# Performance work log

Hardware: AMD Instinct MI355X
Metric: run time of the kernel (lower is better)

Reference implementation:

```python
import jax, jax.numpy as jnp
import numpy as np

EPS = 1e-5

def _ln(t, g, b):
    m = t.mean(-1, keepdims=True)
    v = ((t - m) ** 2).mean(-1, keepdims=True)
    return (t - m) * jax.lax.rsqrt(v + EPS) * g + b

def _sr(t, w, b, H, W, sr):
    # t: [B, H*W, C] -> spatial-reduction conv -> [B, (H//sr)*(W//sr), C]
    B, L, C = t.shape
    xi = t.transpose(0, 2, 1).reshape(B, C, H, W)
    y = jax.lax.conv_general_dilated(xi, w, (sr, sr), 'VALID',
                                     dimension_numbers=('NCHW', 'OIHW', 'NCHW'))
    return y.reshape(B, C, -1).transpose(0, 2, 1) + b

def setup_inputs() -> dict:
    key = jax.random.key(0)
    ks = jax.random.split(key, 9)
    C, head, sr, H, W = 128, 2, 2, 64, 64
    B, N = 4, 2 * H * W
    s = 0.02
    return {
        'x': jax.random.normal(ks[0], (B, N, C), jnp.float32),
        'qW': jax.random.normal(ks[1], (C, C), jnp.float32) * s,
        'qb': jnp.zeros((C,), jnp.float32),
        'kvW': jax.random.normal(ks[2], (C, 2 * C), jnp.float32) * s,
        'kvb': jnp.zeros((2 * C,), jnp.float32),
        'projW': jax.random.normal(ks[3], (C, C), jnp.float32) * s,
        'projb': jnp.zeros((C,), jnp.float32),
        'srW': jax.random.normal(ks[4], (C, C, sr, sr), jnp.float32) * s,
        'srb': jnp.zeros((C,), jnp.float32),
        'lnW': jnp.ones((C,), jnp.float32),
        'lnB': jnp.zeros((C,), jnp.float32),
        'H': H, 'W': W, 'fuse': 1,
    }

def reference(x, qW, qb, kvW, kvb, projW, projb, srW, srb, lnW, lnB, H, W, fuse):
    head, sr = 2, 2
    B, N, C = x.shape
    Dh = C // head
    scale = Dh ** -0.5
    q = (x @ qW + qb).reshape(B, N, head, Dh).transpose(0, 2, 1, 3)  # [B,h,N,Dh]
    mask = None
    if fuse and sr > 1:
        half = N // 2
        x_rgb = _ln(_sr(x[:, :half, :], srW, srb, H, W, sr), lnW, lnB)
        x_dte = _ln(_sr(x[:, half:, :], srW, srb, H, W, sr), lnW, lnB)
        xkv = jnp.concatenate([x_rgb, x_dte], axis=1)
        M = N // (sr * sr)
        row = jnp.arange(N)[:, None] < half            # query in rgb half
        col = jnp.arange(M)[None, :] < (M // 2)        # key in rgb half
        mask = row == col                              # True on same-modality blocks -> masked
    elif sr > 1:
        xkv = _ln(_sr(x, srW, srb, H, W, sr), lnW, lnB)
    else:
        xkv = x
    M = xkv.shape[1]
    kv = (xkv @ kvW + kvb).reshape(B, M, 2, head, Dh).transpose(2, 0, 3, 1, 4)
    k, v = kv[0], kv[1]                                # [B,h,M,Dh]
    attn = jnp.einsum('bhnd,bhmd->bhnm', q, k) * scale
    if mask is not None:
        attn = jnp.where(mask[None, None], -jnp.inf, attn)
    attn = jax.nn.softmax(attn, axis=-1)
    out = jnp.einsum('bhnm,bhmd->bhnd', attn, v).transpose(0, 2, 1, 3).reshape(B, N, C)
    return out @ projW + projb
```

## Files before the change

### kernel.cpp

```cpp
#include <hip/hip_runtime.h>
#include <hip/hip_bf16.h>

#define LN_EPS 1e-5f

typedef __attribute__((ext_vector_type(8))) short bf16x8_t;
typedef __attribute__((ext_vector_type(4))) float f32x4_t;
typedef __attribute__((ext_vector_type(4))) unsigned short u16x4_t;

#define MFMA32(a, b, c) __builtin_amdgcn_mfma_f32_16x16x32_bf16(a, b, c, 0, 0, 0)

__device__ inline float fast_exp2(float x) {
#if __has_builtin(__builtin_amdgcn_exp2f)
    return __builtin_amdgcn_exp2f(x);
#else
    float r;
    asm volatile("v_exp_f32 %0, %1\n\ts_nop 0" : "=v"(r) : "v"(x));
    return r;
#endif
}

__device__ inline unsigned short f2bf(float f) {
    union { float f; unsigned int u; } v; v.f = f;
    unsigned int r = v.u + 0x7fffu + ((v.u >> 16) & 1u);
    return (unsigned short)(r >> 16);
}

__device__ inline u16x4_t pk4(float a, float b, float c, float d) {
    union { u16x4_t v; __hip_bfloat162 h[2]; } u;
    u.h[0] = __float22bfloat162_rn(float2{a, b});
    u.h[1] = __float22bfloat162_rn(float2{c, d});
    return u.v;
}
__device__ inline bf16x8_t pk8(float4 a, float4 b) {
    union { bf16x8_t v; __hip_bfloat162 h[4]; } u;
    u.h[0] = __float22bfloat162_rn(float2{a.x, a.y});
    u.h[1] = __float22bfloat162_rn(float2{a.z, a.w});
    u.h[2] = __float22bfloat162_rn(float2{b.x, b.y});
    u.h[3] = __float22bfloat162_rn(float2{b.z, b.w});
    return u.v;
}

__device__ inline size_t fragidx(int row, int k, int KC) {
    return ((size_t)((row >> 4) * KC + (k >> 5))) * 512 +
           (((k >> 3) & 3) * 16 + (row & 15)) * 8 + (k & 7);
}

__global__ void k_prep_w(const float* __restrict__ qW, const float* __restrict__ kvW,
                         const float* __restrict__ projW, const float* __restrict__ srW,
                         unsigned short* __restrict__ qWs, unsigned short* __restrict__ kvWs,
                         unsigned short* __restrict__ projWs, unsigned short* __restrict__ srWs) {
    int i = blockIdx.x * 256 + threadIdx.x;
    if (i < 16384) {
        int n = i & 127, k = i >> 7;
        qWs[fragidx(n, k, 4)] = f2bf(qW[k * 128 + n]);
    } else if (i < 49152) {
        int j = i - 16384; int n = j & 255, k = j >> 8;
        kvWs[fragidx(n, k, 4)] = f2bf(kvW[k * 256 + n]);
    } else if (i < 65536) {
        int j = i - 49152; int n = j & 127, k = j >> 7;
        projWs[fragidx(n, k, 4)] = f2bf(projW[k * 128 + n]);
    } else {
        int j = i - 65536; int n = j >> 9, rem = j & 511, q = rem >> 7, c = rem & 127;
        srWs[fragidx(n, q * 128 + c, 16)] = f2bf(srW[n * 512 + c * 4 + q]);
    }
}

#define XPAD 132
__global__ __launch_bounds__(256)
void k_convkv(const float* __restrict__ x, const unsigned short* __restrict__ srWs,
              const float* __restrict__ srb, const float* __restrict__ lnW,
              const float* __restrict__ lnB, const unsigned short* __restrict__ kvWs,
              const float* __restrict__ kvb, unsigned short* __restrict__ ksw,
              unsigned short* __restrict__ vls) {
    const int t = threadIdx.x, w = t >> 6, lane = t & 63;
    const int col = lane & 15, quad = lane >> 4;
    const int RT = blockIdx.x;

    __shared__ unsigned short xl[64 * XPAD];
    __shared__ unsigned short xs[4 * 512];
    __shared__ float lnred[4][16][2];

    const int pb = RT >> 7, phf = (RT >> 6) & 1;
    const int oy = (RT >> 1) & 31, ox0 = (RT & 1) * 16;
    const int n0 = phf * 4096 + 2 * oy * 64 + 2 * ox0;
    #pragma unroll
    for (int it = 0; it < 8; it++) {
        int idx = it * 256 + t;
        int chunk = idx >> 10;
        int rr = (idx >> 5) & 31;
        int c4 = idx & 31;
        float4 v = *(const float4*)(x + ((size_t)(pb * 8192 + n0 + chunk * 64 + rr)) * 128 + c4 * 4);
        *(u16x4_t*)(xl + (chunk * 32 + rr) * XPAD + c4 * 4) = pk4(v.x, v.y, v.z, v.w);
    }
    __syncthreads();

    f32x4_t acc[2] = {};
    {
        const unsigned short* wp = srWs + lane * 8;
        #pragma unroll
        for (int kc = 0; kc < 16; kc++) {
            const int q = kc >> 2, cg = kc & 3;
            const int r = (q >> 1) * 32 + 2 * col + (q & 1);
            bf16x8_t xb = *(const bf16x8_t*)(xl + r * XPAD + cg * 32 + quad * 8);
            #pragma unroll
            for (int jj = 0; jj < 2; jj++) {
                bf16x8_t wf = *(const bf16x8_t*)(wp + (size_t)((w * 2 + jj) * 16 + kc) * 512);
                acc[jj] = MFMA32(wf, xb, acc[jj]);
            }
        }
    }
    float s = 0.f, ss = 0.f;
    #pragma unroll
    for (int jj = 0; jj < 2; jj++) {
        float4 bs = *(const float4*)(srb + (w * 2 + jj) * 16 + quad * 4);
        acc[jj][0] += bs.x; acc[jj][1] += bs.y; acc[jj][2] += bs.z; acc[jj][3] += bs.w;
        #pragma unroll
        for (int r = 0; r < 4; r++) { float v = acc[jj][r]; s += v; ss += v * v; }
    }
    s += __shfl_xor(s, 16, 64);  s += __shfl_xor(s, 32, 64);
    ss += __shfl_xor(ss, 16, 64); ss += __shfl_xor(ss, 32, 64);
    if (lane < 16) { lnred[w][lane][0] = s; lnred[w][lane][1] = ss; }
    __syncthreads();
    float stot = 0.f, sstot = 0.f;
    #pragma unroll
    for (int ww = 0; ww < 4; ww++) { stot += lnred[ww][col][0]; sstot += lnred[ww][col][1]; }
    float mean = stot * (1.0f / 128.0f);
    float var = sstot * (1.0f / 128.0f) - mean * mean;
    float rs = rsqrtf(var + LN_EPS);
    #pragma unroll
    for (int jj = 0; jj < 2; jj++) {
        int f0 = (w * 2 + jj) * 16 + quad * 4;
        float4 g = *(const float4*)(lnW + f0);
        float4 be = *(const float4*)(lnB + f0);
        u16x4_t o = pk4((acc[jj][0] - mean) * rs * g.x + be.x,
                        (acc[jj][1] - mean) * rs * g.y + be.y,
                        (acc[jj][2] - mean) * rs * g.z + be.z,
                        (acc[jj][3] - mean) * rs * g.w + be.w);
        *(u16x4_t*)(xs + ((size_t)(f0 >> 5)) * 512 +
                    (((f0 >> 3) & 3) * 16 + col) * 8 + (f0 & 7)) = o;
    }
    __syncthreads();
    bf16x8_t xf[4];
    #pragma unroll
    for (int kc = 0; kc < 4; kc++)
        xf[kc] = *(const bf16x8_t*)(xs + (size_t)kc * 512 + lane * 8);
    const int p0 = RT * 16;
    const int bb = p0 >> 11;
    #pragma unroll
    for (int jj = 0; jj < 2; jj++) {
        const int nt = w * 2 + jj;
        f32x4_t aK = {};
        #pragma unroll
        for (int kc = 0; kc < 4; kc++) {
            bf16x8_t wf = *(const bf16x8_t*)(kvWs + (size_t)(nt * 4 + kc) * 512 + lane * 8);
            aK = MFMA32(wf, xf[kc], aK);
        }
        float4 bs = *(const float4*)(kvb + nt * 16 + quad * 4);
        int m = (p0 + col) & 2047;
        int bh = bb * 2 + (nt >> 2);
        int d0 = (nt & 3) * 16 + quad * 4;
        u16x4_t o = pk4(aK[0] + bs.x, aK[1] + bs.y, aK[2] + bs.z, aK[3] + bs.w);
        *(u16x4_t*)(ksw + ((size_t)(bh * 128 + (m >> 4)) * 2 + (d0 >> 5)) * 512 +
                    (((d0 >> 3) & 3) * 16 + (m & 15)) * 8 + (d0 & 7)) = o;
    }
    #pragma unroll
    for (int jj = 0; jj < 2; jj++) {
        const int nt = w * 2 + jj;
        f32x4_t aV = {};
        #pragma unroll
        for (int kc = 0; kc < 4; kc++) {
            bf16x8_t wf = *(const bf16x8_t*)(kvWs + (size_t)((8 + nt) * 4 + kc) * 512 + lane * 8);
            aV = MFMA32(xf[kc], wf, aV);
        }
        int fv = nt * 16 + col;
        int h = fv >> 6, dd = fv & 63;
        float bv = kvb[128 + fv];
        int m0 = (p0 + quad * 4) & 2047;
        int bh = bb * 2 + h;
        int kt = m0 >> 6;
        int tt = (m0 >> 5) & 1;
        int base = m0 & 31;
        int quad_b = base >> 3, j0 = base & 7;
        u16x4_t o = pk4(aV[0] + bv, aV[1] + bv, aV[2] + bv, aV[3] + bv);
        *(u16x4_t*)(vls + (((size_t)((bh * 32 + kt) * 4 + (dd >> 4)) * 2 + tt) * 512) +
                    (quad_b * 16 + (dd & 15)) * 8 + j0) = o;
    }
}

__global__ __launch_bounds__(256, 2)
void k_attn_f7(const float* __restrict__ x, const unsigned short* __restrict__ qWs,
               const float* __restrict__ qb, const unsigned short* __restrict__ ksw,
               const unsigned short* __restrict__ vls, const unsigned short* __restrict__ projWs,
               const float* __restrict__ projb, float* __restrict__ out) {
    const int blkx = blockIdx.x, mod = blockIdx.y, b = blockIdx.z;
    const int t = threadIdx.x, w = t >> 6, lane = t & 63;
    const int col = lane & 15, quad = lane >> 4;
    const int qg = w & 1, h = w >> 1;
    const int bh = b * 2 + h;
    const int qbase = mod * 4096 + blkx * 64 + qg * 32;

    __shared__ unsigned short sbuf[64 * 136];
    __shared__ unsigned short pls[4][2048];

    unsigned short* qarea = sbuf + w * 2048;
    const float sc = 0.125f * 1.44269504089f;
    #pragma unroll
    for (int qt = 0; qt < 2; qt++) {
        const float* xrow = x + ((size_t)b * 8192 + qbase + qt * 16 + col) * 128;
        f32x4_t acc[4] = {};
        #pragma unroll
        for (int kc = 0; kc < 4; kc++) {
            float4 xa = *(const float4*)(xrow + kc * 32 + quad * 8);
            float4 xb2 = *(const float4*)(xrow + kc * 32 + quad * 8 + 4);
            bf16x8_t xf = pk8(xa, xb2);
            #pragma unroll
            for (int j = 0; j < 4; j++) {
                bf16x8_t wf = *(const bf16x8_t*)(qWs + (size_t)((h * 4 + j) * 4 + kc) * 512 + lane * 8);
                acc[j] = MFMA32(wf, xf, acc[j]);
            }
        }
        #pragma unroll
        for (int j = 0; j < 4; j++) {
            float4 bs = *(const float4*)(qb + h * 64 + j * 16 + quad * 4);
            u16x4_t o = pk4((acc[j][0] + bs.x) * sc, (acc[j][1] + bs.y) * sc,
                            (acc[j][2] + bs.z) * sc, (acc[j][3] + bs.w) * sc);
            *(u16x4_t*)(qarea + ((size_t)(qt * 2 + (j >> 1))) * 512 +
                        (((j & 1) * 2 + (quad >> 1)) * 16 + col) * 8 + (quad & 1) * 4) = o;
        }
    }
    bf16x8_t qf[2][2];
    #pragma unroll
    for (int qt = 0; qt < 2; qt++)
        #pragma unroll
        for (int kc = 0; kc < 2; kc++)
            qf[qt][kc] = *(const bf16x8_t*)(qarea + (size_t)(qt * 2 + kc) * 512 + lane * 8);
    __syncthreads();

    const unsigned short* kp0 =
        ksw + ((size_t)(bh * 128 + (1 - mod) * 64) * 2) * 512 + lane * 8;
    const unsigned short* vp0 =
        vls + ((size_t)((bh * 32 + (1 - mod) * 16) * 8)) * 512 + lane * 8;
    const bf16x8_t ones8 = { 0x3F80, 0x3F80, 0x3F80, 0x3F80,
                             0x3F80, 0x3F80, 0x3F80, 0x3F80 };
    unsigned short* parea = pls[w];

    f32x4_t O[2][4] = {};
    f32x4_t accl[2] = {};

    bf16x8_t kf0[8], kf1[8], vf0[8], vf1[8];

    auto pref0 = [&](int kt) {
        #pragma unroll
        for (int i = 0; i < 8; i++) {
            kf0[i] = *(const bf16x8_t*)(kp0 + (size_t)(kt * 8 + i) * 512);
            vf0[i] = *(const bf16x8_t*)(vp0 + (size_t)(kt * 8 + i) * 512);
        }
    };
    auto pref1 = [&](int kt) {
        #pragma unroll
        for (int i = 0; i < 8; i++) {
            kf1[i] = *(const bf16x8_t*)(kp0 + (size_t)(kt * 8 + i) * 512);
            vf1[i] = *(const bf16x8_t*)(vp0 + (size_t)(kt * 8 + i) * 512);
        }
    };
    auto body = [&](bf16x8_t (&kfc)[8], bf16x8_t (&vfc)[8]) {
        f32x4_t ST[2][4];
        #pragma unroll
        for (int qt = 0; qt < 2; qt++)
            #pragma unroll
            for (int nb = 0; nb < 4; nb++) {
                f32x4_t sA = {};
                sA = MFMA32(kfc[nb * 2 + 0], qf[qt][0], sA);
                sA = MFMA32(kfc[nb * 2 + 1], qf[qt][1], sA);
                ST[qt][nb] = sA;
            }
        #pragma unroll
        for (int qt = 0; qt < 2; qt++)
            #pragma unroll
            for (int nb = 0; nb < 4; nb++) {
                u16x4_t pk = pk4(fast_exp2(ST[qt][nb][0]), fast_exp2(ST[qt][nb][1]),
                                 fast_exp2(ST[qt][nb][2]), fast_exp2(ST[qt][nb][3]));
                *(u16x4_t*)(parea + qt * 1024 + (nb >> 1) * 512 +
                            (((nb & 1) * 2 + (quad >> 1)) * 16 + col) * 8 + (quad & 1) * 4) = pk;
            }
        bf16x8_t pf[2][2];
        #pragma unroll
        for (int qt = 0; qt < 2; qt++) {
            pf[qt][0] = *(const bf16x8_t*)(parea + qt * 1024 + lane * 8);
            pf[qt][1] = *(const bf16x8_t*)(parea + qt * 1024 + 512 + lane * 8);
        }
        #pragma unroll
        for (int qt = 0; qt < 2; qt++) {
            accl[qt] = MFMA32(pf[qt][0], ones8, accl[qt]);
            accl[qt] = MFMA32(pf[qt][1], ones8, accl[qt]);
            #pragma unroll
            for (int dt = 0; dt < 4; dt++) {
                O[qt][dt] = MFMA32(pf[qt][0], vfc[dt * 2 + 0], O[qt][dt]);
                O[qt][dt] = MFMA32(pf[qt][1], vfc[dt * 2 + 1], O[qt][dt]);
            }
        }
    };

    pref0(0);
    #pragma unroll
    for (int kt2 = 0; kt2 < 8; kt2++) {
        pref1(kt2 * 2 + 1);
        body(kf0, vf0);
        if (kt2 < 7) pref0(kt2 * 2 + 2);
        body(kf1, vf1);
    }

    #pragma unroll
    for (int qt = 0; qt < 2; qt++) {
        #pragma unroll
        for (int r = 0; r < 4; r++) {
            float rl = 1.0f / accl[qt][r];
            int qrow = qg * 32 + qt * 16 + quad * 4 + r;
            #pragma unroll
            for (int dt = 0; dt < 4; dt++)
                sbuf[qrow * 136 + h * 64 + dt * 16 + col] = f2bf(O[qt][dt][r] * rl);
        }
    }
    __syncthreads();
    {
        const int qt2 = w;
        bf16x8_t ob[4];
        #pragma unroll
        for (int kc = 0; kc < 4; kc++)
            ob[kc] = *(const bf16x8_t*)(sbuf + (size_t)(qt2 * 16 + col) * 136 + kc * 32 + quad * 8);
        f32x4_t acc[8];
        #pragma unroll
        for (int j = 0; j < 8; j++) acc[j] = f32x4_t{};
        #pragma unroll
        for (int kc = 0; kc < 4; kc++)
            #pragma unroll
            for (int j = 0; j < 8; j++) {
                bf16x8_t wf = *(const bf16x8_t*)(projWs + (size_t)(j * 4 + kc) * 512 + lane * 8);
                acc[j] = MFMA32(wf, ob[kc], acc[j]);
            }
        const int n = b * 8192 + mod * 4096 + blkx * 64 + qt2 * 16 + col;
        #pragma unroll
        for (int j = 0; j < 8; j++) {
            int f0 = j * 16 + quad * 4;
            float4 bs = *(const float4*)(projb + f0);
            float4 o = { acc[j][0] + bs.x, acc[j][1] + bs.y,
                         acc[j][2] + bs.z, acc[j][3] + bs.w };
            *(float4*)(out + (size_t)n * 128 + f0) = o;
        }
    }
}

extern "C" void kernel_launch(void* const* d_in, const int* in_sizes, int n_in,
                              void* d_out, int out_size, void* d_ws, size_t ws_size,
                              hipStream_t stream) {
    const float* x     = (const float*)d_in[0];
    const float* qW    = (const float*)d_in[1];
    const float* qb    = (const float*)d_in[2];
    const float* kvW   = (const float*)d_in[3];
    const float* kvb   = (const float*)d_in[4];
    const float* projW = (const float*)d_in[5];
    const float* projb = (const float*)d_in[6];
    const float* srW   = (const float*)d_in[7];
    const float* srb   = (const float*)d_in[8];
    const float* lnW   = (const float*)d_in[9];
    const float* lnB   = (const float*)d_in[10];

    char* ws = (char*)d_ws;
    unsigned short* qWs    = (unsigned short*)(ws + 0);
    unsigned short* kvWs   = (unsigned short*)(ws + 32768);
    unsigned short* projWs = (unsigned short*)(ws + 98304);
    unsigned short* srWs   = (unsigned short*)(ws + 131072);
    unsigned short* ksw    = (unsigned short*)(ws + 262144);
    unsigned short* vls    = (unsigned short*)(ws + 2359296);

    k_prep_w<<<dim3(512), dim3(256), 0, stream>>>(qW, kvW, projW, srW,
                                                  qWs, kvWs, projWs, srWs);
    k_convkv<<<dim3(512), dim3(256), 0, stream>>>(x, srWs, srb, lnW, lnB,
                                                  kvWs, kvb, ksw, vls);
    k_attn_f7<<<dim3(64, 2, 4), dim3(256), 0, stream>>>(x, qWs, qb, ksw, vls,
                                                        projWs, projb, (float*)d_out);
}
```

Before: 132.3 us.

## Split key range across warps and combine partial attention outputs in LDS

Each warp now processes all 64 queries of its block for one head, but only half of the key tiles, instead of 32 queries over all keys. The two partial outputs and row sums are merged through shared memory before normalisation and the output projection. This halves the K/V fragment loads per warp and reuses each loaded K/V tile across twice as many queries. In exchange it drops the explicit double-buffered prefetch, adds LDS traffic and extra barriers for the merge, and raises register and LDS use, which may lower occupancy.

```diff
diff --git a/kernel.cpp b/kernel.cpp
--- a/kernel.cpp
+++ b/kernel.cpp
@@ -188,24 +188,26 @@
 }
 
 __global__ __launch_bounds__(256, 2)
-void k_attn_f7(const float* __restrict__ x, const unsigned short* __restrict__ qWs,
+void k_attn_f8(const float* __restrict__ x, const unsigned short* __restrict__ qWs,
                const float* __restrict__ qb, const unsigned short* __restrict__ ksw,
                const unsigned short* __restrict__ vls, const unsigned short* __restrict__ projWs,
                const float* __restrict__ projb, float* __restrict__ out) {
     const int blkx = blockIdx.x, mod = blockIdx.y, b = blockIdx.z;
     const int t = threadIdx.x, w = t >> 6, lane = t & 63;
     const int col = lane & 15, quad = lane >> 4;
-    const int qg = w & 1, h = w >> 1;
+    const int ks = w & 1, h = w >> 1;
     const int bh = b * 2 + h;
-    const int qbase = mod * 4096 + blkx * 64 + qg * 32;
+    const int qbase = mod * 4096 + blkx * 64;
 
     __shared__ unsigned short sbuf[64 * 136];
-    __shared__ unsigned short pls[4][2048];
-
-    unsigned short* qarea = sbuf + w * 2048;
+    __shared__ unsigned short pls[4][4096];
+    __shared__ float Ocomb[64 * 68];
+    __shared__ float lcomb[64];
+
     const float sc = 0.125f * 1.44269504089f;
     #pragma unroll
-    for (int qt = 0; qt < 2; qt++) {
+    for (int qtl = 0; qtl < 2; qtl++) {
+        const int qt = ks * 2 + qtl;
         const float* xrow = x + ((size_t)b * 8192 + qbase + qt * 16 + col) * 128;
         f32x4_t acc[4] = {};
         #pragma unroll
@@ -224,16 +226,18 @@
             float4 bs = *(const float4*)(qb + h * 64 + j * 16 + quad * 4);
             u16x4_t o = pk4((acc[j][0] + bs.x) * sc, (acc[j][1] + bs.y) * sc,
                             (acc[j][2] + bs.z) * sc, (acc[j][3] + bs.w) * sc);
-            *(u16x4_t*)(qarea + ((size_t)(qt * 2 + (j >> 1))) * 512 +
+            *(u16x4_t*)(sbuf + (size_t)h * 4096 + ((size_t)(qt * 2 + (j >> 1))) * 512 +
                         (((j & 1) * 2 + (quad >> 1)) * 16 + col) * 8 + (quad & 1) * 4) = o;
         }
     }
-    bf16x8_t qf[2][2];
-    #pragma unroll
-    for (int qt = 0; qt < 2; qt++)
+    __syncthreads();
+    bf16x8_t qf[4][2];
+    #pragma unroll
+    for (int qt = 0; qt < 4; qt++)
         #pragma unroll
         for (int kc = 0; kc < 2; kc++)
-            qf[qt][kc] = *(const bf16x8_t*)(qarea + (size_t)(qt * 2 + kc) * 512 + lane * 8);
+            qf[qt][kc] = *(const bf16x8_t*)(sbuf + (size_t)h * 4096 +
+                                            (size_t)(qt * 2 + kc) * 512 + lane * 8);
     __syncthreads();
 
     const unsigned short* kp0 =
@@ -244,84 +248,89 @@
                              0x3F80, 0x3F80, 0x3F80, 0x3F80 };
     unsigned short* parea = pls[w];
 
-    f32x4_t O[2][4] = {};
-    f32x4_t accl[2] = {};
-
-    bf16x8_t kf0[8], kf1[8], vf0[8], vf1[8];
-
-    auto pref0 = [&](int kt) {
+    f32x4_t O[4][4] = {};
+    f32x4_t accl[4] = {};
+
+    for (int kti = 0; kti < 8; kti++) {
+        const int kt = ks * 8 + kti;
+        bf16x8_t kf[8], vf[8];
         #pragma unroll
         for (int i = 0; i < 8; i++) {
-            kf0[i] = *(const bf16x8_t*)(kp0 + (size_t)(kt * 8 + i) * 512);
-            vf0[i] = *(const bf16x8_t*)(vp0 + (size_t)(kt * 8 + i) * 512);
-        }
-    };
-    auto pref1 = [&](int kt) {
-        #pragma unroll
-        for (int i = 0; i < 8; i++) {
-            kf1[i] = *(const bf16x8_t*)(kp0 + (size_t)(kt * 8 + i) * 512);
-            vf1[i] = *(const bf16x8_t*)(vp0 + (size_t)(kt * 8 + i) * 512);
-        }
-    };
-    auto body = [&](bf16x8_t (&kfc)[8], bf16x8_t (&vfc)[8]) {
-        f32x4_t ST[2][4];
-        #pragma unroll
-        for (int qt = 0; qt < 2; qt++)
-            #pragma unroll
-            for (int nb = 0; nb < 4; nb++) {
-                f32x4_t sA = {};
-                sA = MFMA32(kfc[nb * 2 + 0], qf[qt][0], sA);
-                sA = MFMA32(kfc[nb * 2 + 1], qf[qt][1], sA);
-                ST[qt][nb] = sA;
-            }
-        #pragma unroll
-        for (int qt = 0; qt < 2; qt++)
-            #pragma unroll
-            for (int nb = 0; nb < 4; nb++) {
-                u16x4_t pk = pk4(fast_exp2(ST[qt][nb][0]), fast_exp2(ST[qt][nb][1]),
-                                 fast_exp2(ST[qt][nb][2]), fast_exp2(ST[qt][nb][3]));
-                *(u16x4_t*)(parea + qt * 1024 + (nb >> 1) * 512 +
-                            (((nb & 1) * 2 + (quad >> 1)) * 16 + col) * 8 + (quad & 1) * 4) = pk;
-            }
-        bf16x8_t pf[2][2];
-        #pragma unroll
-        for (int qt = 0; qt < 2; qt++) {
-            pf[qt][0] = *(const bf16x8_t*)(parea + qt * 1024 + lane * 8);
-            pf[qt][1] = *(const bf16x8_t*)(parea + qt * 1024 + 512 + lane * 8);
-        }
-        #pragma unroll
-        for (int qt = 0; qt < 2; qt++) {
-            accl[qt] = MFMA32(pf[qt][0], ones8, accl[qt]);
-            accl[qt] = MFMA32(pf[qt][1], ones8, accl[qt]);
-            #pragma unroll
-            for (int dt = 0; dt < 4; dt++) {
-                O[qt][dt] = MFMA32(pf[qt][0], vfc[dt * 2 + 0], O[qt][dt]);
-                O[qt][dt] = MFMA32(pf[qt][1], vfc[dt * 2 + 1], O[qt][dt]);
-            }
-        }
-    };
-
-    pref0(0);
-    #pragma unroll
-    for (int kt2 = 0; kt2 < 8; kt2++) {
-        pref1(kt2 * 2 + 1);
-        body(kf0, vf0);
-        if (kt2 < 7) pref0(kt2 * 2 + 2);
-        body(kf1, vf1);
-    }
-
-    #pragma unroll
-    for (int qt = 0; qt < 2; qt++) {
-        #pragma unroll
-        for (int r = 0; r < 4; r++) {
-            float rl = 1.0f / accl[qt][r];
-            int qrow = qg * 32 + qt * 16 + quad * 4 + r;
-            #pragma unroll
-            for (int dt = 0; dt < 4; dt++)
-                sbuf[qrow * 136 + h * 64 + dt * 16 + col] = f2bf(O[qt][dt][r] * rl);
-        }
-    }
-    __syncthreads();
+            kf[i] = *(const bf16x8_t*)(kp0 + (size_t)(kt * 8 + i) * 512);
+            vf[i] = *(const bf16x8_t*)(vp0 + (size_t)(kt * 8 + i) * 512);
+        }
+        #pragma unroll
+        for (int qp = 0; qp < 2; qp++) {
+            f32x4_t ST[2][4];
+            #pragma unroll
+            for (int qtl = 0; qtl < 2; qtl++) {
+                const int qt = qp * 2 + qtl;
+                #pragma unroll
+                for (int nb = 0; nb < 4; nb++) {
+                    f32x4_t sA = {};
+                    sA = MFMA32(kf[nb * 2 + 0], qf[qt][0], sA);
+                    sA = MFMA32(kf[nb * 2 + 1], qf[qt][1], sA);
+                    ST[qtl][nb] = sA;
+                }
+            }
+            #pragma unroll
+            for (int qtl = 0; qtl < 2; qtl++)
+                #pragma unroll
+                for (int nb = 0; nb < 4; nb++) {
+                    u16x4_t pk = pk4(fast_exp2(ST[qtl][nb][0]), fast_exp2(ST[qtl][nb][1]),
+                                     fast_exp2(ST[qtl][nb][2]), fast_exp2(ST[qtl][nb][3]));
+                    *(u16x4_t*)(parea + (qp * 2 + qtl) * 1024 + (nb >> 1) * 512 +
+                                (((nb & 1) * 2 + (quad >> 1)) * 16 + col) * 8 + (quad & 1) * 4) = pk;
+                }
+            #pragma unroll
+            for (int qtl = 0; qtl < 2; qtl++) {
+                const int qt = qp * 2 + qtl;
+                bf16x8_t pf0 = *(const bf16x8_t*)(parea + qt * 1024 + lane * 8);
+                bf16x8_t pf1 = *(const bf16x8_t*)(parea + qt * 1024 + 512 + lane * 8);
+                accl[qt] = MFMA32(pf0, ones8, accl[qt]);
+                accl[qt] = MFMA32(pf1, ones8, accl[qt]);
+                #pragma unroll
+                for (int dt = 0; dt < 4; dt++) {
+                    O[qt][dt] = MFMA32(pf0, vf[dt * 2 + 0], O[qt][dt]);
+                    O[qt][dt] = MFMA32(pf1, vf[dt * 2 + 1], O[qt][dt]);
+                }
+            }
+        }
+    }
+
+    #pragma unroll
+    for (int hp = 0; hp < 2; hp++) {
+        if (h == hp && ks == 1) {
+            #pragma unroll
+            for (int qt = 0; qt < 4; qt++)
+                #pragma unroll
+                for (int r = 0; r < 4; r++) {
+                    int qrow = qt * 16 + quad * 4 + r;
+                    #pragma unroll
+                    for (int dt = 0; dt < 4; dt++)
+                        Ocomb[qrow * 68 + dt * 16 + col] = O[qt][dt][r];
+                    if (col == 0) lcomb[qrow] = accl[qt][r];
+                }
+        }
+        __syncthreads();
+        if (h == hp && ks == 0) {
+            #pragma unroll
+            for (int qt = 0; qt < 4; qt++)
+                #pragma unroll
+                for (int r = 0; r < 4; r++) {
+                    int qrow = qt * 16 + quad * 4 + r;
+                    float lt = accl[qt][r] + lcomb[qrow];
+                    float rl = 1.0f / lt;
+                    #pragma unroll
+                    for (int dt = 0; dt < 4; dt++) {
+                        float ov = O[qt][dt][r] + Ocomb[qrow * 68 + dt * 16 + col];
+                        sbuf[qrow * 136 + hp * 64 + dt * 16 + col] = f2bf(ov * rl);
+                    }
+                }
+        }
+        __syncthreads();
+    }
+
     {
         const int qt2 = w;
         bf16x8_t ob[4];
@@ -338,7 +347,7 @@
                 bf16x8_t wf = *(const bf16x8_t*)(projWs + (size_t)(j * 4 + kc) * 512 + lane * 8);
                 acc[j] = MFMA32(wf, ob[kc], acc[j]);
             }
-        const int n = b * 8192 + mod * 4096 + blkx * 64 + qt2 * 16 + col;
+        const int n = b * 8192 + qbase + qt2 * 16 + col;
         #pragma unroll
         for (int j = 0; j < 8; j++) {
             int f0 = j * 16 + quad * 4;
@@ -377,6 +386,6 @@
                                                   qWs, kvWs, projWs, srWs);
     k_convkv<<<dim3(512), dim3(256), 0, stream>>>(x, srWs, srb, lnW, lnB,
                                                   kvWs, kvb, ksw, vls);
-    k_attn_f7<<<dim3(64, 2, 4), dim3(256), 0, stream>>>(x, qWs, qb, ksw, vls,
+    k_attn_f8<<<dim3(64, 2, 4), dim3(256), 0, stream>>>(x, qWs, qb, ksw, vls,
                                                         projWs, projb, (float*)d_out);
 }
```

Result: faster. 129.2 us (-2.4%).
